# Optimization experiments

Measured on AMD Instinct MI355X. Metric: run time of the kernel, lower is better.

The kernel has to match this reference:

```python
import jax, jax.numpy as jnp
import numpy as np

B, N, D = 64, 128, 512
NEG = 1e30


def _gru_cell(x, h, Wi, Wh, bi, bh):
    # torch nn.GRUCell math
    gi = x @ Wi.T + bi  # (B, 3D)
    gh = h @ Wh.T + bh  # (B, 3D)
    ir, iz, inn = jnp.split(gi, 3, axis=-1)
    hr, hz, hn = jnp.split(gh, 3, axis=-1)
    r = jax.nn.sigmoid(ir + hr)
    z = jax.nn.sigmoid(iz + hz)
    n = jnp.tanh(inn + r * hn)
    return (1.0 - z) * n + z * h


def setup_inputs() -> dict:
    key = jax.random.key(0)
    ks = jax.random.split(key, 16)
    s = 1.0 / np.sqrt(D)
    u = lambda k, shape: jax.random.uniform(k, shape, jnp.float32, -s, s)
    adj = jax.random.randint(ks[13], (B, N, N), 0, 2, jnp.int32)
    adj = adj.at[:, :, 0].set(1)  # ensure each causal prefix has >=1 unmasked edge
    s_mask = jax.random.randint(ks[14], (B, N, N), 0, 2, jnp.int32)
    o_mask = 1 - s_mask
    return {
        "features": jax.random.normal(ks[0], (B, N, D), jnp.float32),
        "Wi_c": u(ks[1], (3 * D, D)),
        "Wh_c": u(ks[2], (3 * D, D)),
        "bi_c": u(ks[3], (3 * D,)),
        "bh_c": u(ks[4], (3 * D,)),
        "Wi_p": u(ks[5], (3 * D, D)),
        "Wh_p": u(ks[6], (3 * D, D)),
        "bi_p": u(ks[7], (3 * D,)),
        "bh_p": u(ks[8], (3 * D,)),
        "lin_w": u(ks[9], (1, 2 * D)),
        "lin_b": u(ks[10], (1,)),
        "Wr0": u(ks[11], (D, D)),
        "Wr1": u(ks[12], (D, D)),
        "adj": adj,
        "s_mask": s_mask,
        "o_mask": o_mask,
    }


def reference(features, Wi_c, Wh_c, bi_c, bh_c, Wi_p, Wh_p, bi_p, bh_p,
              lin_w, lin_b, Wr0, Wr1, adj, s_mask, o_mask):
    dt = features.dtype
    adj_f = adj.astype(dt)
    s_f = s_mask.astype(dt)
    o_f = o_mask.astype(dt)
    wq = lin_w[0, :D]   # applies to Q half of cat(Q, K)
    wk = lin_w[0, D:]   # applies to K half
    b = lin_b[0]
    pos = jnp.arange(N)

    # step 0
    x0 = features[:, 0]
    zeros = jnp.zeros((B, D), dt)
    C0 = _gru_cell(x0, zeros, Wi_c, Wh_c, bi_c, bh_c)
    P0 = _gru_cell(zeros, x0, Wi_p, Wh_p, bi_p, bh_p)
    H0 = jnp.zeros((B, N, D), dt).at[:, 0].set(C0 + P0)

    def step(H, inputs):
        i, x, adj_row, s_row, o_row = inputs
        # masked graph attention over the causal prefix [0, i)
        alpha = (x @ wq)[:, None] + H @ wk + b          # (B, N)
        valid = adj_row * (pos < i).astype(dt)          # (B, N)
        alpha = alpha - (1.0 - valid) * NEG
        w = jax.nn.softmax(alpha, axis=1)               # (B, N)
        V = (H @ Wr0.T) * s_row[:, :, None] + (H @ Wr1.T) * o_row[:, :, None]
        M = jnp.einsum('bn,bnd->bd', w, V)              # (B, D)
        C = _gru_cell(x, M, Wi_c, Wh_c, bi_c, bh_c)
        P = _gru_cell(M, x, Wi_p, Wh_p, bi_p, bh_p)
        H = H.at[:, i].set(C + P)
        return H, None

    xs = (jnp.arange(1, N),
          jnp.swapaxes(features, 0, 1)[1:],
          jnp.swapaxes(adj_f, 0, 1)[1:],
          jnp.swapaxes(s_f, 0, 1)[1:],
          jnp.swapaxes(o_f, 0, 1)[1:])
    H1, _ = jax.lax.scan(step, H0, xs)
    return H1
```

## Files before the change

kernel.cpp:

```cpp
#include <hip/hip_runtime.h>

#define BB 64
#define NN 128
#define DD 512
#define NBLK 128
#define NTHR 512
#define GCOLS 24
#define WCS 2064
#define WXS 1032
#define BCS 6656
#define UBE (BB * 2048)

typedef unsigned short u16;
typedef unsigned int u32;
typedef unsigned long long u64;
typedef __attribute__((ext_vector_type(8))) __bf16 bf16x8;
typedef __attribute__((ext_vector_type(4))) float f32x4;

#define MFMA16(a, b, c) __builtin_amdgcn_mfma_f32_16x16x32_bf16((a), (b), (c), 0, 0, 0)

__device__ __forceinline__ float b2f(u16 u) {
    union { u32 i; float f; } c; c.i = ((u32)u) << 16; return c.f;
}
__device__ __forceinline__ u16 f2b(float f) {
    union { float f; u32 i; } c; c.f = f;
    return (u16)((c.i + 0x7FFFu + ((c.i >> 16) & 1u)) >> 16);
}
__device__ __forceinline__ float sigm(float x) { return 1.f / (1.f + __expf(-x)); }
__device__ __forceinline__ float tanh_(float x) {
    x = fminf(fmaxf(x, -15.f), 15.f);
    float e = __expf(2.f * x);
    return (e - 1.f) / (e + 1.f);
}

__device__ __forceinline__ float ld_cohf(const float* p) {
    return __hip_atomic_load((float*)p, __ATOMIC_RELAXED, __HIP_MEMORY_SCOPE_AGENT);
}
__device__ __forceinline__ void st_cohf(float* p, float v) {
    __hip_atomic_store(p, v, __ATOMIC_RELAXED, __HIP_MEMORY_SCOPE_AGENT);
}
__device__ __forceinline__ void st_cohu32(u32* p, u32 v) {
    __hip_atomic_store(p, v, __ATOMIC_RELAXED, __HIP_MEMORY_SCOPE_AGENT);
}
__device__ __forceinline__ void st_cohi(int* p, int v) {
    __hip_atomic_store(p, v, __ATOMIC_RELAXED, __HIP_MEMORY_SCOPE_AGENT);
}
__device__ __forceinline__ int ld_cohi(int* p) {
    return __hip_atomic_load(p, __ATOMIC_RELAXED, __HIP_MEMORY_SCOPE_AGENT);
}

template<bool CACHED>
__device__ __forceinline__ bf16x8 ldu16(const u16* p) {
    if constexpr (CACHED) {
        return *(const bf16x8*)p;
    } else {
        union { bf16x8 v; u64 q[2]; } u;
        u.q[0] = __hip_atomic_load((u64*)p,     __ATOMIC_RELAXED, __HIP_MEMORY_SCOPE_AGENT);
        u.q[1] = __hip_atomic_load((u64*)p + 1, __ATOMIC_RELAXED, __HIP_MEMORY_SCOPE_AGENT);
        return u.v;
    }
}

__device__ __forceinline__ void gbar(int* sync, int gen, int blk) {
    __syncthreads();
    int* epoch = sync;
    if (blk == 0) {
        const int t = threadIdx.x;
        int done = (t == 0 || t >= NBLK) ? 1 : 0;
        int* myarr = sync + 256 + t * 16;
        int it = 0;
        for (;;) {
            if (!done) {
                int v = ((it & 15) == 15)
                    ? __hip_atomic_load(myarr, __ATOMIC_ACQUIRE, __HIP_MEMORY_SCOPE_AGENT)
                    : __hip_atomic_load(myarr, __ATOMIC_RELAXED, __HIP_MEMORY_SCOPE_AGENT);
                done = (v >= gen);
            }
            ++it;
            if (__syncthreads_and(done)) break;
            __builtin_amdgcn_s_sleep(1);
        }
        if (t == 0) {
            (void)__hip_atomic_load(sync + 256 + 16, __ATOMIC_ACQUIRE, __HIP_MEMORY_SCOPE_AGENT);
            __hip_atomic_store(epoch, gen, __ATOMIC_RELEASE, __HIP_MEMORY_SCOPE_AGENT);
        }
        __syncthreads();
    } else {
        if (threadIdx.x == 0) {
            __hip_atomic_store(sync + 256 + blk * 16, gen, __ATOMIC_RELEASE, __HIP_MEMORY_SCOPE_AGENT);
            int it = 0;
            for (;;) {
                int v = ((it & 15) == 15)
                    ? __hip_atomic_load(epoch, __ATOMIC_ACQUIRE, __HIP_MEMORY_SCOPE_AGENT)
                    : __hip_atomic_load(epoch, __ATOMIC_RELAXED, __HIP_MEMORY_SCOPE_AGENT);
                ++it;
                if (v >= gen) break;
                __builtin_amdgcn_s_sleep(1);
            }
            (void)__hip_atomic_load(epoch, __ATOMIC_ACQUIRE, __HIP_MEMORY_SCOPE_AGENT);
        }
        __syncthreads();
    }
}

__device__ __forceinline__ void gbar_lite(int* flags, int gen, int blk,
                                          int nsig, bool sig, bool wait) {
    __syncthreads();
    if (sig && threadIdx.x == 0)
        st_cohi(flags + blk * 32, gen);
    if (wait) {
        const int t = threadIdx.x;
        int done = (t >= nsig) ? 1 : 0;
        int* f = flags + t * 32;
        for (;;) {
            if (!done) done = (ld_cohi(f) >= gen);
            if (__syncthreads_and(done)) break;
            __builtin_amdgcn_s_sleep(2);
        }
    }
    asm volatile("" ::: "memory");
    __builtin_amdgcn_sched_barrier(0);
}

__device__ __forceinline__ void waitA(int* flagsA, int gen, int grp) {
    const int l = threadIdx.x & 63;
    int* f = flagsA + (grp * 16 + (l & 15)) * 32;
    for (;;) {
        int v = ld_cohi(f);
        if (__all(v >= gen)) break;
        __builtin_amdgcn_s_sleep(1);
    }
    asm volatile("" ::: "memory");
    __builtin_amdgcn_sched_barrier(0);
}

template<bool CACHED>
__device__ __forceinline__ void gates_merged(
    const u16* __restrict__ ub, const u16* s_wc, const float* s_gb,
    float* __restrict__ bc, int blk, int rt, int lr, int lq)
{
    const int cc0 = lr, cc1 = lr + 8;
    const u16* w0 = s_wc + cc0 * WCS;
    const u16* w1 = s_wc + cc1 * WCS;
    const u16* arow = ub + (size_t)(rt * 16 + lr) * 2048;
    f32x4 acc0 = {0.f, 0.f, 0.f, 0.f}, acc1 = {0.f, 0.f, 0.f, 0.f};
    #pragma unroll 4
    for (int c = 0; c < 16; ++c) {
        int kk = c * 32 + lq * 8;
        bf16x8 ah = ldu16<CACHED>(arow + kk);
        bf16x8 al = ldu16<CACHED>(arow + 512 + kk);
        bf16x8 wh0 = *(const bf16x8*)(w0 + kk);
        bf16x8 wl0 = *(const bf16x8*)(w0 + 1024 + kk);
        bf16x8 wh1 = *(const bf16x8*)(w1 + kk);
        bf16x8 wl1 = *(const bf16x8*)(w1 + 1024 + kk);
        acc0 = MFMA16(ah, wh0, acc0); acc0 = MFMA16(al, wh0, acc0); acc0 = MFMA16(ah, wl0, acc0);
        acc1 = MFMA16(ah, wh1, acc1); acc1 = MFMA16(al, wh1, acc1); acc1 = MFMA16(ah, wl1, acc1);
    }
    #pragma unroll 4
    for (int c = 0; c < 16; ++c) {
        int kk = c * 32 + lq * 8;
        bf16x8 ah = ldu16<CACHED>(arow + 1024 + kk);
        bf16x8 al = ldu16<CACHED>(arow + 1536 + kk);
        bf16x8 wh0 = *(const bf16x8*)(w0 + 512 + kk);
        bf16x8 wl0 = *(const bf16x8*)(w0 + 1536 + kk);
        bf16x8 wh1 = *(const bf16x8*)(w1 + 512 + kk);
        bf16x8 wl1 = *(const bf16x8*)(w1 + 1536 + kk);
        acc0 = MFMA16(ah, wh0, acc0); acc0 = MFMA16(al, wh0, acc0); acc0 = MFMA16(ah, wl0, acc0);
        acc1 = MFMA16(ah, wh1, acc1); acc1 = MFMA16(al, wh1, acc1); acc1 = MFMA16(ah, wl1, acc1);
    }
    float b0 = s_gb[cc0], b1 = s_gb[cc1];
    int col0 = blk * GCOLS + cc0, col1 = blk * GCOLS + cc1;
    #pragma unroll
    for (int r = 0; r < 4; ++r) {
        size_t row = (size_t)(rt * 16 + lq * 4 + r) * BCS;
        st_cohf(bc + row + 512 + col0, acc0[r] + b0);
        st_cohf(bc + row + 512 + col1, acc1[r] + b1);
    }
}

__device__ __forceinline__ f32x4 x_core(
    int i, const u16* __restrict__ featblob, const u16* s_wxw,
    int task, int lr, int lq, int* ccO)
{
    const int ct = task & 1, rt = task >> 1;
    const int cc = ct * 8 + lr;
    *ccO = cc;
    const u16* wcol = s_wxw + cc * WXS;
    const u16* arow = featblob + (size_t)(i * 64 + rt * 16 + lr) * 1024;
    f32x4 acc = {0.f, 0.f, 0.f, 0.f};
    #pragma unroll 4
    for (int c = 0; c < 16; ++c) {
        int kk = c * 32 + lq * 8;
        bf16x8 ah = *(const bf16x8*)(arow + kk);
        bf16x8 al = *(const bf16x8*)(arow + 512 + kk);
        bf16x8 wh = *(const bf16x8*)(wcol + kk);
        bf16x8 wl = *(const bf16x8*)(wcol + 512 + kk);
        acc = MFMA16(ah, wh, acc); acc = MFMA16(al, wh, acc); acc = MFMA16(ah, wl, acc);
    }
    return acc;
}

__device__ __forceinline__ void x_task(
    int i, const u16* __restrict__ featblob, const u16* s_wxw, const float* s_xb,
    float* __restrict__ bc, int blk, int task, int lr, int lq)
{
    int cc; f32x4 acc = x_core(i, featblob, s_wxw, task, lr, lq, &cc);
    const int rt = task >> 1;
    const int col = blk * GCOLS + cc;
    float bias = s_xb[cc];
    #pragma unroll
    for (int r = 0; r < 4; ++r)
        st_cohf(bc + (size_t)(rt * 16 + lq * 4 + r) * BCS + 3584 + col, acc[r] + bias);
}

__device__ __forceinline__ void x_task_xg(
    int i, const u16* __restrict__ featblob, const u16* s_wxw, const float* s_xb,
    float* __restrict__ xg, int blk, int task, int lr, int lq)
{
    int cc; f32x4 acc = x_core(i, featblob, s_wxw, task, lr, lq, &cc);
    const int rt = task >> 1;
    const int col = blk * GCOLS + cc;
    float bias = s_xb[cc];
    #pragma unroll
    for (int r = 0; r < 4; ++r)
        xg[((size_t)i * 64 + rt * 16 + lq * 4 + r) * 3072 + col] = acc[r] + bias;
}

template<bool CACHED>
__device__ __forceinline__ void m_task(
    const u16* __restrict__ ub, const u16* __restrict__ WrB,
    float* __restrict__ bc, int blk, int lr, int lq)
{
    const int ct = blk >> 2, rt = blk & 3;
    const int col = ct * 16 + lr;
    const u16* wcol = WrB + (size_t)col * 2048;
    const u16* arow = ub + (size_t)(rt * 16 + lr) * 2048;
    f32x4 acc = {0.f, 0.f, 0.f, 0.f};
    #pragma unroll 4
    for (int c = 0; c < 16; ++c) {
        int kk = c * 32 + lq * 8;
        bf16x8 a0h = ldu16<CACHED>(arow + kk);
        bf16x8 a0l = ldu16<CACHED>(arow + 512 + kk);
        bf16x8 a1h = ldu16<CACHED>(arow + 1024 + kk);
        bf16x8 a1l = ldu16<CACHED>(arow + 1536 + kk);
        bf16x8 w0h = *(const bf16x8*)(wcol + kk);
        bf16x8 w0l = *(const bf16x8*)(wcol + 512 + kk);
        bf16x8 w1h = *(const bf16x8*)(wcol + 1024 + kk);
        bf16x8 w1l = *(const bf16x8*)(wcol + 1536 + kk);
        acc = MFMA16(a0h, w0h, acc); acc = MFMA16(a0l, w0h, acc); acc = MFMA16(a0h, w0l, acc);
        acc = MFMA16(a1h, w1h, acc); acc = MFMA16(a1l, w1h, acc); acc = MFMA16(a1h, w1l, acc);
    }
    #pragma unroll
    for (int r = 0; r < 4; ++r)
        st_cohf(bc + (size_t)(rt * 16 + lq * 4 + r) * BCS + col, acc[r]);
}

__global__ __launch_bounds__(NTHR) void grn_kernel(
    const float* __restrict__ feat, const float* __restrict__ Wi_c, const float* __restrict__ Wh_c,
    const float* __restrict__ bi_c, const float* __restrict__ bh_c,
    const float* __restrict__ Wi_p, const float* __restrict__ Wh_p,
    const float* __restrict__ bi_p, const float* __restrict__ bh_p,
    const float* __restrict__ lin_w, const float* __restrict__ lin_b,
    const float* __restrict__ Wr0, const float* __restrict__ Wr1,
    const int* __restrict__ adj, const int* __restrict__ smask,
    float* __restrict__ out,
    float* __restrict__ q, u16* __restrict__ ublob,
    u16* __restrict__ featblob, float* __restrict__ bc, u16* __restrict__ WrB,
    float* __restrict__ xg, int* __restrict__ sync, int use_ring, int use_xg)
{
    const int t = threadIdx.x, blk = blockIdx.x;
    const int lane = t & 63, wv = t >> 6;
    const int lr = lane & 15, lq = lane >> 4;
    int gen = 0;
    int* flagsA = sync + 4096;
    int* flagsB = sync + 8192;

    __shared__ u16 s_wc[GCOLS * WCS];
    __shared__ __align__(16) char s_wx_raw[GCOLS * WXS * 2];
    __shared__ float s_u0[DD];
    __shared__ float s_ut[DD];
    __shared__ float s_red[NTHR];
    __shared__ float s_hk[NN];
    __shared__ float s_q[NN];
    __shared__ float s_w[NN];
    __shared__ float s_ws[NN];
    __shared__ float s_gb[GCOLS];
    __shared__ float s_xb[GCOLS];

    u16* s_wxw = (u16*)s_wx_raw;
    float* s_wgf = (float*)s_wx_raw;
    float* s_pu = (float*)s_wx_raw;
    float* s_pt = (float*)(s_wx_raw + 6144);
    float* s_scal = (float*)(s_wx_raw + 12288);

    const float wkreg = lin_w[DD + t];

    for (int rr = 0; rr < 64; ++rr) {
        int gr = blk * 64 + rr;
        int bb_ = gr >> 7, nn_ = gr & 127;
        float x = feat[(size_t)gr * DD + t];
        u16 h = f2b(x);
        u16* dst = featblob + (size_t)(nn_ * 64 + bb_) * 1024;
        dst[t] = h;
        dst[512 + t] = f2b(x - b2f(h));
    }
    for (int cc = 0; cc < 4; ++cc) {
        int c = blk * 4 + cc;
        float w0 = Wr0[(size_t)c * DD + t], w1 = Wr1[(size_t)c * DD + t];
        u16 h0 = f2b(w0), h1 = f2b(w1);
        u16* dst = WrB + (size_t)c * 2048;
        dst[t] = h0; dst[512 + t] = f2b(w0 - b2f(h0));
        dst[1024 + t] = h1; dst[1536 + t] = f2b(w1 - b2f(h1));
    }
    {
        float linb = lin_b[0];
        float wqf[8];
        #pragma unroll
        for (int jj = 0; jj < 8; ++jj) wqf[jj] = lin_w[lane * 8 + jj];
        for (int rr = 0; rr < 8; ++rr) {
            int row = blk * 64 + wv * 8 + rr;
            const float* fp = feat + (size_t)row * DD + lane * 8;
            float p = 0.f;
            #pragma unroll
            for (int jj = 0; jj < 8; ++jj) p += fp[jj] * wqf[jj];
            #pragma unroll
            for (int off = 32; off; off >>= 1) p += __shfl_down(p, off, 64);
            if (lane == 0) q[row] = p + linb;
        }
    }
    {
        int jg0 = blk * GCOLS;
        for (int cc = 0; cc < GCOLS; ++cc) {
            int jg = jg0 + cc;
            const float* src = (jg < 1536) ? (Wh_c + (size_t)jg * DD) : (Wi_p + (size_t)(jg - 1536) * DD);
            s_wgf[t * GCOLS + cc] = src[t];
        }
        if (t < GCOLS) {
            int jg = jg0 + t;
            s_gb[t] = (jg < 1536) ? bh_c[jg] : bi_p[jg - 1536];
            s_xb[t] = (jg < 1536) ? bi_c[jg] : bh_p[jg - 1536];
        }
    }
    __syncthreads();
    {
        float acc0[GCOLS], acc1[GCOLS];
        #pragma unroll
        for (int cc = 0; cc < GCOLS; ++cc) { acc0[cc] = 0.f; acc1[cc] = 0.f; }
        for (int j = 0; j < DD; ++j) {
            float wr0 = Wr0[(size_t)j * DD + t];
            float wr1 = Wr1[(size_t)j * DD + t];
            const float* g = s_wgf + j * GCOLS;
            #pragma unroll
            for (int cc = 0; cc < GCOLS; ++cc) {
                float gv = g[cc];
                acc0[cc] += wr0 * gv;
                acc1[cc] += wr1 * gv;
            }
        }
        __syncthreads();
        #pragma unroll
        for (int cc = 0; cc < GCOLS; ++cc) {
            u16 h0 = f2b(acc0[cc]);
            s_wc[cc * WCS + t] = h0;
            s_wc[cc * WCS + 1024 + t] = f2b(acc0[cc] - b2f(h0));
            u16 h1 = f2b(acc1[cc]);
            s_wc[cc * WCS + 512 + t] = h1;
            s_wc[cc * WCS + 1536 + t] = f2b(acc1[cc] - b2f(h1));
        }
    }
    {
        int jx0 = blk * GCOLS;
        for (int cc = 0; cc < GCOLS; ++cc) {
            int jx = jx0 + cc;
            const float* src = (jx < 1536) ? (Wi_c + (size_t)jx * DD) : (Wh_p + (size_t)(jx - 1536) * DD);
            float w = src[t];
            u16 h = f2b(w);
            s_wxw[cc * WXS + t] = h;
            s_wxw[cc * WXS + 512 + t] = f2b(w - b2f(h));
        }
    }
    gbar(sync, ++gen, blk);

    x_task(0, featblob, s_wxw, s_xb, bc, blk, wv, lr, lq);
    if (use_xg) {
        for (int ii = 0; ii < NN; ++ii)
            x_task_xg(ii, featblob, s_wxw, s_xb, xg, blk, wv, lr, lq);
    }
    if (blk < BB && t < NN) s_q[t] = q[blk * NN + t];
    gbar(sync, ++gen, blk);

    if (blk < BB) {
        if (use_xg) {
            s_pu[t] = 0.f; s_pu[512 + t] = 0.f; s_pu[1024 + t] = 0.f;
            s_pt[t] = 0.f; s_pt[512 + t] = 0.f; s_pt[1024 + t] = 0.f;
            if (t == 0) {
                s_scal[0] = -1e30f; s_scal[1] = 0.f;
                s_scal[2] = (float)adj[((size_t)blk * NN + 1) * NN + 0];
                s_scal[3] = (float)smask[((size_t)blk * NN + 1) * NN + 0];
            }
        }
        const float* bcb = bc + (size_t)blk * BCS;
        float ir = ld_cohf(bcb + 3584 + t), iz = ld_cohf(bcb + 4096 + t), inn = ld_cohf(bcb + 4608 + t);
        float r = sigm(ir + bh_c[t]), z = sigm(iz + bh_c[512 + t]);
        float C = (1.f - z) * tanh_(inn + r * bh_c[1024 + t]);
        float ghr = ld_cohf(bcb + 5120 + t), ghz = ld_cohf(bcb + 5632 + t), ghn = ld_cohf(bcb + 6144 + t);
        float r2 = sigm(bi_p[t] + ghr), z2 = sigm(bi_p[512 + t] + ghz);
        float n2 = tanh_(bi_p[1024 + t] + r2 * ghn);
        float x = feat[(size_t)(blk * NN) * DD + t];
        float P = (1.f - z2) * n2 + z2 * x;
        float Hv = C + P;
        out[(size_t)(blk * NN) * DD + t] = Hv;
        s_red[t] = Hv * wkreg;
        __syncthreads();
        if (wv == 0) {
            float p = 0.f;
            #pragma unroll
            for (int jj = 0; jj < 8; ++jj) p += s_red[lane + 64 * jj];
            #pragma unroll
            for (int off = 32; off; off >>= 1) p += __shfl_down(p, off, 64);
            if (lane == 0) s_hk[0] = p;
        }
    }
    gbar(sync, ++gen, blk);

    for (int i = 1; i < NN; ++i) {
        u16* ub_i = ublob + (size_t)(use_ring ? (NN - 1 - i) : 0) * UBE;

        if (blk < BB) {
            if (use_xg) {
                int j = i - 1;
                float Hv;
                if (i >= 2) {
                    const float* bcb = bc + (size_t)blk * BCS;
                    float Mv = ld_cohf(bcb + t);
                    float hr = ld_cohf(bcb + 512 + t), hz = ld_cohf(bcb + 1024 + t), hn = ld_cohf(bcb + 1536 + t);
                    float gir = ld_cohf(bcb + 2048 + t), giz = ld_cohf(bcb + 2560 + t), gin = ld_cohf(bcb + 3072 + t);
                    const float* xrow = xg + ((size_t)j * 64 + blk) * 3072;
                    float ir = xrow[t], iz = xrow[512 + t], inn = xrow[1024 + t];
                    float ghr = xrow[1536 + t], ghz = xrow[2048 + t], ghn = xrow[2560 + t];
                    float x = feat[(size_t)(blk * NN + j) * DD + t];
                    float r = sigm(ir + hr), z = sigm(iz + hz);
                    float C = (1.f - z) * tanh_(inn + r * hn) + z * Mv;
                    float r2 = sigm(gir + ghr), z2 = sigm(giz + ghz);
                    float P = (1.f - z2) * tanh_(gin + r2 * ghn) + z2 * x;
                    Hv = C + P;
                    out[(size_t)(blk * NN + j) * DD + t] = Hv;
                    s_red[t] = Hv * wkreg;
                } else {
                    Hv = out[(size_t)(blk * NN) * DD + t];
                }
                __syncthreads();
                if (wv == 0) {
                    float hk;
                    if (i >= 2) {
                        float p = 0.f;
                        #pragma unroll
                        for (int jj = 0; jj < 8; ++jj) p += s_red[lane + 64 * jj];
                        #pragma unroll
                        for (int off = 32; off; off >>= 1) p += __shfl_down(p, off, 64);
                        if (lane == 0) s_hk[j] = p;
                        hk = p;
                    } else {
                        hk = s_hk[0];
                    }
                    if (lane == 0) {
                        float m_part = s_scal[0], denom_p = s_scal[1];
                        float anew = s_scal[2], snew = s_scal[3];
                        float alpha = s_q[i] + hk;
                        float m = m_part, e_new = 0.f;
                        if (anew != 0.f) { m = fmaxf(m_part, alpha); e_new = __expf(alpha - m); }
                        float scale = __expf(m_part - m);
                        float inv = 1.f / (denom_p * scale + e_new);
                        s_w[0] = scale * inv;
                        s_w[1] = e_new * snew * inv;
                        s_w[2] = e_new * inv;
                    }
                }
                __syncthreads();
                {
                    float u0p = s_pu[t] + s_pu[512 + t] + s_pu[1024 + t];
                    float utp = s_pt[t] + s_pt[512 + t] + s_pt[1024 + t];
                    float CS = s_w[0], C0 = s_w[1], CT = s_w[2];
                    float U0 = u0p * CS + C0 * Hv;
                    float U1 = (utp * CS + CT * Hv) - U0;
                    u16 h0 = f2b(U0); u16 l0 = f2b(U0 - b2f(h0));
                    u16 h1 = f2b(U1); u16 l1 = f2b(U1 - b2f(h1));
                    u32 p0 = (u32)h0 | ((u32)l0 << 16);
                    u32 p1 = (u32)h1 | ((u32)l1 << 16);
                    u32 q0 = (u32)__shfl_xor((int)p0, 1, 64);
                    u32 q1 = (u32)__shfl_xor((int)p1, 1, 64);
                    u32* ub32 = (u32*)(ub_i + (size_t)blk * 2048);
                    int w = t >> 1;
                    if ((t & 1) == 0) {
                        st_cohu32(ub32 + w,       (p0 & 0xFFFFu) | ((q0 & 0xFFFFu) << 16));
                        st_cohu32(ub32 + 256 + w, (p0 >> 16)     | (q0 & 0xFFFF0000u));
                    } else {
                        st_cohu32(ub32 + 512 + w, (q1 & 0xFFFFu) | ((p1 & 0xFFFFu) << 16));
                        st_cohu32(ub32 + 768 + w, (q1 >> 16)     | (p1 & 0xFFFF0000u));
                    }
                }
                __syncthreads();
                if (t == 0) st_cohi(flagsA + blk * 32, i);
            } else {
                int va0 = 0, va1 = 0, vs0 = 0, vs1 = 0;
                float qv = 0.f;
                if (wv == 0) {
                    const int* ar_ = adj + (size_t)(blk * NN + i) * NN;
                    const int* sr_ = smask + (size_t)(blk * NN + i) * NN;
                    va0 = ar_[lane]; va1 = ar_[lane + 64];
                    vs0 = sr_[lane]; vs1 = sr_[lane + 64];
                    qv = s_q[i];
                }
                if (i >= 2) {
                    int j = i - 1;
                    const float* bcb = bc + (size_t)blk * BCS;
                    float Mv = ld_cohf(bcb + t);
                    float hr = ld_cohf(bcb + 512 + t), hz = ld_cohf(bcb + 1024 + t), hn = ld_cohf(bcb + 1536 + t);
                    float gir = ld_cohf(bcb + 2048 + t), giz = ld_cohf(bcb + 2560 + t), gin = ld_cohf(bcb + 3072 + t);
                    float ir = ld_cohf(bcb + 3584 + t), iz = ld_cohf(bcb + 4096 + t), inn = ld_cohf(bcb + 4608 + t);
                    float ghr = ld_cohf(bcb + 5120 + t), ghz = ld_cohf(bcb + 5632 + t), ghn = ld_cohf(bcb + 6144 + t);
                    float x = feat[(size_t)(blk * NN + j) * DD + t];
                    float r = sigm(ir + hr), z = sigm(iz + hz);
                    float C = (1.f - z) * tanh_(inn + r * hn) + z * Mv;
                    float r2 = sigm(gir + ghr), z2 = sigm(giz + ghz);
                    float P = (1.f - z2) * tanh_(gin + r2 * ghn) + z2 * x;
                    float Hv = C + P;
                    out[(size_t)(blk * NN + j) * DD + t] = Hv;
                    s_red[t] = Hv * wkreg;
                }
                s_u0[t] = 0.f; s_ut[t] = 0.f;
                __syncthreads();
                if (wv == 0) {
                    if (i >= 2) {
                        float p = 0.f;
                        #pragma unroll
                        for (int jj = 0; jj < 8; ++jj) p += s_red[lane + 64 * jj];
                        #pragma unroll
                        for (int off = 32; off; off >>= 1) p += __shfl_down(p, off, 64);
                        if (lane == 0) s_hk[i - 1] = p;
                    }
                    int n2i = lane + 64;
                    float a0 = (lane < i && va0 != 0) ? (qv + s_hk[lane]) : -1e30f;
                    float a1 = (n2i < i && va1 != 0) ? (qv + s_hk[n2i]) : -1e30f;
                    float m = fmaxf(a0, a1);
                    #pragma unroll
                    for (int off = 32; off; off >>= 1) m = fmaxf(m, __shfl_xor(m, off, 64));
                    float e0 = (a0 > -1e29f) ? __expf(a0 - m) : 0.f;
                    float e1 = (a1 > -1e29f) ? __expf(a1 - m) : 0.f;
                    float ss = e0 + e1;
                    #pragma unroll
                    for (int off = 32; off; off >>= 1) ss += __shfl_xor(ss, off, 64);
                    float inv = 1.f / ss;
                    float w0 = e0 * inv, w1 = e1 * inv;
                    s_w[lane] = w0; s_w[n2i] = w1;
                    s_ws[lane] = w0 * (float)vs0;
                    s_ws[n2i] = w1 * (float)vs1;
                }
                __syncthreads();
                {
                    int g = t >> 7, dqb = (t & 127) * 4;
                    const float* Hb = out + (size_t)blk * NN * DD + dqb;
                    f32x4 u0 = {0.f, 0.f, 0.f, 0.f}, ut = {0.f, 0.f, 0.f, 0.f};
                    int n = g;
                    for (; n + 12 < i; n += 16) {
                        f32x4 h0 = *(const f32x4*)(Hb + (size_t)n * DD);
                        f32x4 h1 = *(const f32x4*)(Hb + (size_t)(n + 4) * DD);
                        f32x4 h2 = *(const f32x4*)(Hb + (size_t)(n + 8) * DD);
                        f32x4 h3 = *(const f32x4*)(Hb + (size_t)(n + 12) * DD);
                        u0 += s_ws[n] * h0 + s_ws[n + 4] * h1 + s_ws[n + 8] * h2 + s_ws[n + 12] * h3;
                        ut += s_w[n] * h0 + s_w[n + 4] * h1 + s_w[n + 8] * h2 + s_w[n + 12] * h3;
                    }
                    for (; n < i; n += 4) {
                        f32x4 h0 = *(const f32x4*)(Hb + (size_t)n * DD);
                        u0 += s_ws[n] * h0;
                        ut += s_w[n] * h0;
                    }
                    #pragma unroll
                    for (int e = 0; e < 4; ++e) {
                        atomicAdd(&s_u0[dqb + e], u0[e]);
                        atomicAdd(&s_ut[dqb + e], ut[e]);
                    }
                }
                __syncthreads();
                {
                    int tt = t & 255, sel = t >> 8;
                    float a0 = s_u0[2 * tt], a1 = s_u0[2 * tt + 1];
                    float t0_ = s_ut[2 * tt], t1_ = s_ut[2 * tt + 1];
                    float b0_ = t0_ - a0, b1_ = t1_ - a1;
                    float v0 = sel ? b0_ : a0, v1 = sel ? b1_ : a1;
                    u16 h0 = f2b(v0), h1 = f2b(v1);
                    u16 l0 = f2b(v0 - b2f(h0)), l1 = f2b(v1 - b2f(h1));
                    u32 hw = (u32)h0 | ((u32)h1 << 16);
                    u32 lw = (u32)l0 | ((u32)l1 << 16);
                    u32* ub32 = (u32*)(ub_i + (size_t)blk * 2048);
                    int base = sel * 512;
                    st_cohu32(ub32 + base + tt, hw);
                    st_cohu32(ub32 + base + 256 + tt, lw);
                }
                __syncthreads();
                if (t == 0) st_cohi(flagsA + blk * 32, i);
            }
        }

        if (use_xg) {
            if (wv < 4) {
                waitA(flagsA, i, wv);
                if (use_ring) gates_merged<true >(ub_i, s_wc, s_gb, bc, blk, wv, lr, lq);
                else          gates_merged<false>(ub_i, s_wc, s_gb, bc, blk, wv, lr, lq);
            } else if (wv == 7) {
                waitA(flagsA, i, blk & 3);
                if (use_ring) m_task<true >(ub_i, WrB, bc, blk, lr, lq);
                else          m_task<false>(ub_i, WrB, bc, blk, lr, lq);
            } else if (blk < BB && i + 1 < NN) {
                const int ii = i + 1;
                const int w = wv - 4;
                const int* ar = adj + (size_t)(blk * NN + ii) * NN;
                const int* sr = smask + (size_t)(blk * NN + ii) * NN;
                int a0 = ar[lane], a1 = ar[lane + 64];
                int s0 = sr[lane], s1 = sr[lane + 64];
                float qv = s_q[ii];
                float al0 = (lane < i && a0 != 0) ? (qv + s_hk[lane]) : -1e30f;
                float al1 = (lane + 64 < i && a1 != 0) ? (qv + s_hk[lane + 64]) : -1e30f;
                float m = fmaxf(al0, al1);
                #pragma unroll
                for (int off = 32; off; off >>= 1) m = fmaxf(m, __shfl_xor(m, off, 64));
                float e0 = (al0 > -1e29f) ? __expf(al0 - m) : 0.f;
                float e1 = (al1 > -1e29f) ? __expf(al1 - m) : 0.f;
                float es0 = e0 * (float)s0, es1 = e1 * (float)s1;
                const float* Hb = out + (size_t)blk * NN * DD + lane * 8;
                f32x4 pa = {0.f,0.f,0.f,0.f}, pb = {0.f,0.f,0.f,0.f};
                f32x4 ta = {0.f,0.f,0.f,0.f}, tb = {0.f,0.f,0.f,0.f};
                for (int n = w; n < i; n += 3) {
                    float en  = __shfl((n < 64) ? e0 : e1, n & 63, 64);
                    float esn = __shfl((n < 64) ? es0 : es1, n & 63, 64);
                    f32x4 h0 = *(const f32x4*)(Hb + (size_t)n * DD);
                    f32x4 h1 = *(const f32x4*)(Hb + (size_t)n * DD + 4);
                    pa += esn * h0; pb += esn * h1;
                    ta += en * h0;  tb += en * h1;
                }
                *(f32x4*)&s_pu[w * 512 + lane * 8]     = pa;
                *(f32x4*)&s_pu[w * 512 + lane * 8 + 4] = pb;
                *(f32x4*)&s_pt[w * 512 + lane * 8]     = ta;
                *(f32x4*)&s_pt[w * 512 + lane * 8 + 4] = tb;
                if (w == 0) {
                    float ds = e0 + e1;
                    #pragma unroll
                    for (int off = 32; off; off >>= 1) ds += __shfl_xor(ds, off, 64);
                    if (lane == 0) {
                        s_scal[0] = m; s_scal[1] = ds;
                        s_scal[2] = (float)ar[i];
                        s_scal[3] = (float)sr[i];
                    }
                }
                if (w == 2) {
                    const float* fp = feat + (size_t)(blk * NN + i) * DD + lane * 8;
                    f32x4 f0 = *(const f32x4*)fp;
                    f32x4 f1 = *(const f32x4*)(fp + 4);
                    const float* xp = xg + ((size_t)i * 64 + blk) * 3072 + lane * 16;
                    float x0 = xp[0], x1 = xp[1024], x2 = xp[2048];
                    asm volatile("" :: "v"(f0), "v"(f1), "v"(x0), "v"(x1), "v"(x2));
                }
            }
        } else {
            if (wv < 4) {
                waitA(flagsA, i, wv);
                gates_merged<false>(ub_i, s_wc, s_gb, bc, blk, wv, lr, lq);
            } else if (wv == 4) {
                x_task(i, featblob, s_wxw, s_xb, bc, blk, 0, lr, lq);
                x_task(i, featblob, s_wxw, s_xb, bc, blk, 1, lr, lq);
                x_task(i, featblob, s_wxw, s_xb, bc, blk, 2, lr, lq);
            } else if (wv == 5) {
                x_task(i, featblob, s_wxw, s_xb, bc, blk, 3, lr, lq);
                x_task(i, featblob, s_wxw, s_xb, bc, blk, 4, lr, lq);
                x_task(i, featblob, s_wxw, s_xb, bc, blk, 5, lr, lq);
            } else if (wv == 6) {
                x_task(i, featblob, s_wxw, s_xb, bc, blk, 6, lr, lq);
                x_task(i, featblob, s_wxw, s_xb, bc, blk, 7, lr, lq);
            } else {
                waitA(flagsA, i, blk & 3);
                m_task<false>(ub_i, WrB, bc, blk, lr, lq);
            }
        }

        gbar_lite(flagsB, i, blk, NBLK, true, blk < BB);
    }

    if (blk < BB) {
        int j = NN - 1;
        const float* bcb = bc + (size_t)blk * BCS;
        float Mv = ld_cohf(bcb + t);
        float hr = ld_cohf(bcb + 512 + t), hz = ld_cohf(bcb + 1024 + t), hn = ld_cohf(bcb + 1536 + t);
        float gir = ld_cohf(bcb + 2048 + t), giz = ld_cohf(bcb + 2560 + t), gin = ld_cohf(bcb + 3072 + t);
        float ir, iz, inn, ghr, ghz, ghn;
        if (use_xg) {
            const float* xrow = xg + ((size_t)j * 64 + blk) * 3072;
            ir = xrow[t]; iz = xrow[512 + t]; inn = xrow[1024 + t];
            ghr = xrow[1536 + t]; ghz = xrow[2048 + t]; ghn = xrow[2560 + t];
        } else {
            ir = ld_cohf(bcb + 3584 + t); iz = ld_cohf(bcb + 4096 + t); inn = ld_cohf(bcb + 4608 + t);
            ghr = ld_cohf(bcb + 5120 + t); ghz = ld_cohf(bcb + 5632 + t); ghn = ld_cohf(bcb + 6144 + t);
        }
        float x = feat[(size_t)(blk * NN + j) * DD + t];
        float r = sigm(ir + hr), z = sigm(iz + hz);
        float C = (1.f - z) * tanh_(inn + r * hn) + z * Mv;
        float r2 = sigm(gir + ghr), z2 = sigm(giz + ghz);
        float P = (1.f - z2) * tanh_(gin + r2 * ghn) + z2 * x;
        out[(size_t)(blk * NN + j) * DD + t] = C + P;
    }
}

extern "C" void kernel_launch(void* const* d_in, const int* in_sizes, int n_in,
                              void* d_out, int out_size, void* d_ws, size_t ws_size,
                              hipStream_t stream) {
    (void)in_sizes; (void)n_in; (void)out_size;
    const float* feat = (const float*)d_in[0];
    const float* Wi_c = (const float*)d_in[1];
    const float* Wh_c = (const float*)d_in[2];
    const float* bi_c = (const float*)d_in[3];
    const float* bh_c = (const float*)d_in[4];
    const float* Wi_p = (const float*)d_in[5];
    const float* Wh_p = (const float*)d_in[6];
    const float* bi_p = (const float*)d_in[7];
    const float* bh_p = (const float*)d_in[8];
    const float* lin_w = (const float*)d_in[9];
    const float* lin_b = (const float*)d_in[10];
    const float* Wr0 = (const float*)d_in[11];
    const float* Wr1 = (const float*)d_in[12];
    const int* adj = (const int*)d_in[13];
    const int* smask = (const int*)d_in[14];
    float* out = (float*)d_out;

    char* ws = (char*)d_ws;
    size_t off = 0;
    int* sync_ = (int*)(ws + off);      off += 65536;
    float* q = (float*)(ws + off);      off += (size_t)BB * NN * 4;
    u16* featblob = (u16*)(ws + off);   off += (size_t)BB * NN * 1024 * 2;
    float* bc = (float*)(ws + off);     off += (size_t)BB * BCS * 4;
    u16* WrB = (u16*)(ws + off);        off += (size_t)512 * 2048 * 2;
    u16* ublob = (u16*)(ws + off);
    size_t ring_bytes = (size_t)(NN - 1) * UBE * 2;
    size_t xg_bytes = (size_t)NN * 64 * 3072 * 4;
    int use_ring = (ws_size >= off + ring_bytes) ? 1 : 0;
    float* xg = (float*)(ws + off + ring_bytes);
    int use_xg = (use_ring && ws_size >= off + ring_bytes + xg_bytes) ? 1 : 0;

    (void)hipMemsetAsync(d_ws, 0, 65536, stream);
    hipLaunchKernelGGL(grn_kernel, dim3(NBLK), dim3(NTHR), 0, stream,
                       feat, Wi_c, Wh_c, bi_c, bh_c, Wi_p, Wh_p, bi_p, bh_p,
                       lin_w, lin_b, Wr0, Wr1, adj, smask, out,
                       q, ublob, featblob, bc, WrB, xg, sync_, use_ring, use_xg);
}
```

Baseline: 3.418 ms.

## Replace per-step grid barrier with per-wave completion counters and flag waits

On the precomputed-x path, the end-of-step grid barrier is removed. Each gate/M wave now bumps a shared-memory counter after its stores drain, and the last of the five raises a per-block flag. Consumer blocks wait at the start of the next step until all 128 producer flags reach the previous step. This lets the attention-prep waves of the next step overlap with other waves still running gate work, and cuts full-barrier overhead. The cost is more complex memory-ordering and flag logic, plus a risk of races if the counter thresholds or visibility are wrong.

After: 3.419 ms. About the same (+0.0%).

```diff
diff --git a/kernel.cpp b/kernel.cpp
--- a/kernel.cpp
+++ b/kernel.cpp
@@ -134,6 +134,15 @@
     __builtin_amdgcn_sched_barrier(0);
 }
 
+__device__ __forceinline__ void sigB(int* flagsB, int* sd, int i, int blk, int lane) {
+    asm volatile("s_waitcnt vmcnt(0)" ::: "memory");
+    if (lane == 0) {
+        int old = atomicAdd(sd, 1);
+        if (old == 5 * i - 1)
+            st_cohi(flagsB + blk * 32, i);
+    }
+}
+
 template<bool CACHED>
 __device__ __forceinline__ void gates_merged(
     const u16* __restrict__ ub, const u16* s_wc, const float* s_gb,
@@ -143,7 +152,7 @@
     const u16* w0 = s_wc + cc0 * WCS;
     const u16* w1 = s_wc + cc1 * WCS;
     const u16* arow = ub + (size_t)(rt * 16 + lr) * 2048;
-    f32x4 acc0 = {0.f, 0.f, 0.f, 0.f}, acc1 = {0.f, 0.f, 0.f, 0.f};
+    f32x4 acc0 = {0.f,0.f,0.f,0.f}, acc1 = {0.f,0.f,0.f,0.f};
     #pragma unroll 4
     for (int c = 0; c < 16; ++c) {
         int kk = c * 32 + lq * 8;
@@ -187,7 +196,7 @@
     *ccO = cc;
     const u16* wcol = s_wxw + cc * WXS;
     const u16* arow = featblob + (size_t)(i * 64 + rt * 16 + lr) * 1024;
-    f32x4 acc = {0.f, 0.f, 0.f, 0.f};
+    f32x4 acc = {0.f,0.f,0.f,0.f};
     #pragma unroll 4
     for (int c = 0; c < 16; ++c) {
         int kk = c * 32 + lq * 8;
@@ -235,7 +244,7 @@
     const int col = ct * 16 + lr;
     const u16* wcol = WrB + (size_t)col * 2048;
     const u16* arow = ub + (size_t)(rt * 16 + lr) * 2048;
-    f32x4 acc = {0.f, 0.f, 0.f, 0.f};
+    f32x4 acc = {0.f,0.f,0.f,0.f};
     #pragma unroll 4
     for (int c = 0; c < 16; ++c) {
         int kk = c * 32 + lq * 8;
@@ -286,6 +295,7 @@
     __shared__ float s_ws[NN];
     __shared__ float s_gb[GCOLS];
     __shared__ float s_xb[GCOLS];
+    __shared__ int s_done;
 
     u16* s_wxw = (u16*)s_wx_raw;
     float* s_wgf = (float*)s_wx_raw;
@@ -421,13 +431,29 @@
             if (lane == 0) s_hk[0] = p;
         }
     }
+    if (t == 0) s_done = 0;
     gbar(sync, ++gen, blk);
 
     for (int i = 1; i < NN; ++i) {
         u16* ub_i = ublob + (size_t)(use_ring ? (NN - 1 - i) : 0) * UBE;
 
-        if (blk < BB) {
-            if (use_xg) {
+        if (use_xg) {
+            if (blk < BB) {
+                if (i >= 2) {
+                    if (wv == 0) {
+                        int* fa = flagsB + lane * 32;
+                        int* fb = flagsB + (lane + 64) * 32;
+                        for (;;) {
+                            int va = ld_cohi(fa);
+                            int vb = ld_cohi(fb);
+                            if (__all((va >= i - 1) && (vb >= i - 1))) break;
+                            __builtin_amdgcn_s_sleep(1);
+                        }
+                        asm volatile("" ::: "memory");
+                        __builtin_amdgcn_sched_barrier(0);
+                    }
+                    __syncthreads();
+                }
                 int j = i - 1;
                 float Hv;
                 if (i >= 2) {
@@ -501,7 +527,82 @@
                 }
                 __syncthreads();
                 if (t == 0) st_cohi(flagsA + blk * 32, i);
+
+                if (wv < 4) {
+                    waitA(flagsA, i, wv);
+                    if (use_ring) gates_merged<true >(ub_i, s_wc, s_gb, bc, blk, wv, lr, lq);
+                    else          gates_merged<false>(ub_i, s_wc, s_gb, bc, blk, wv, lr, lq);
+                    sigB(flagsB, &s_done, i, blk, lane);
+                } else if (wv == 7) {
+                    waitA(flagsA, i, blk & 3);
+                    if (use_ring) m_task<true >(ub_i, WrB, bc, blk, lr, lq);
+                    else          m_task<false>(ub_i, WrB, bc, blk, lr, lq);
+                    sigB(flagsB, &s_done, i, blk, lane);
+                } else if (i + 1 < NN) {
+                    const int ii = i + 1;
+                    const int w = wv - 4;
+                    const int* ar = adj + (size_t)(blk * NN + ii) * NN;
+                    const int* sr = smask + (size_t)(blk * NN + ii) * NN;
+                    int a0 = ar[lane], a1 = ar[lane + 64];
+                    int s0 = sr[lane], s1 = sr[lane + 64];
+                    float qv = s_q[ii];
+                    float al0 = (lane < i && a0 != 0) ? (qv + s_hk[lane]) : -1e30f;
+                    float al1 = (lane + 64 < i && a1 != 0) ? (qv + s_hk[lane + 64]) : -1e30f;
+                    float m = fmaxf(al0, al1);
+                    #pragma unroll
+                    for (int off = 32; off; off >>= 1) m = fmaxf(m, __shfl_xor(m, off, 64));
+                    float e0 = (al0 > -1e29f) ? __expf(al0 - m) : 0.f;
+                    float e1 = (al1 > -1e29f) ? __expf(al1 - m) : 0.f;
+                    float es0 = e0 * (float)s0, es1 = e1 * (float)s1;
+                    const float* Hb = out + (size_t)blk * NN * DD + lane * 8;
+                    f32x4 pa = {0.f,0.f,0.f,0.f}, pb = {0.f,0.f,0.f,0.f};
+                    f32x4 ta = {0.f,0.f,0.f,0.f}, tb = {0.f,0.f,0.f,0.f};
+                    for (int n = w; n < i; n += 3) {
+                        float en  = __shfl((n < 64) ? e0 : e1, n & 63, 64);
+                        float esn = __shfl((n < 64) ? es0 : es1, n & 63, 64);
+                        f32x4 h0 = *(const f32x4*)(Hb + (size_t)n * DD);
+                        f32x4 h1 = *(const f32x4*)(Hb + (size_t)n * DD + 4);
+                        pa += esn * h0; pb += esn * h1;
+                        ta += en * h0;  tb += en * h1;
+                    }
+                    *(f32x4*)&s_pu[w * 512 + lane * 8]     = pa;
+                    *(f32x4*)&s_pu[w * 512 + lane * 8 + 4] = pb;
+                    *(f32x4*)&s_pt[w * 512 + lane * 8]     = ta;
+                    *(f32x4*)&s_pt[w * 512 + lane * 8 + 4] = tb;
+                    if (w == 0) {
+                        float ds = e0 + e1;
+                        #pragma unroll
+                        for (int off = 32; off; off >>= 1) ds += __shfl_xor(ds, off, 64);
+                        if (lane == 0) {
+                            s_scal[0] = m; s_scal[1] = ds;
+                            s_scal[2] = (float)ar[i];
+                            s_scal[3] = (float)sr[i];
+                        }
+                    }
+                    if (w == 2) {
+                        const float* fp = feat + (size_t)(blk * NN + i) * DD + lane * 8;
+                        f32x4 f0 = *(const f32x4*)fp;
+                        f32x4 f1 = *(const f32x4*)(fp + 4);
+                        const float* xp = xg + ((size_t)i * 64 + blk) * 3072 + lane * 16;
+                        float x0 = xp[0], x1 = xp[1024], x2 = xp[2048];
+                        asm volatile("" :: "v"(f0), "v"(f1), "v"(x0), "v"(x1), "v"(x2));
+                    }
+                }
             } else {
+                if (wv < 4) {
+                    waitA(flagsA, i, wv);
+                    if (use_ring) gates_merged<true >(ub_i, s_wc, s_gb, bc, blk, wv, lr, lq);
+                    else          gates_merged<false>(ub_i, s_wc, s_gb, bc, blk, wv, lr, lq);
+                    sigB(flagsB, &s_done, i, blk, lane);
+                } else if (wv == 7) {
+                    waitA(flagsA, i, blk & 3);
+                    if (use_ring) m_task<true >(ub_i, WrB, bc, blk, lr, lq);
+                    else          m_task<false>(ub_i, WrB, bc, blk, lr, lq);
+                    sigB(flagsB, &s_done, i, blk, lane);
+                }
+            }
+        } else {
+            if (blk < BB) {
                 int va0 = 0, va1 = 0, vs0 = 0, vs1 = 0;
                 float qv = 0.f;
                 if (wv == 0) {
@@ -560,7 +661,7 @@
                 {
                     int g = t >> 7, dqb = (t & 127) * 4;
                     const float* Hb = out + (size_t)blk * NN * DD + dqb;
-                    f32x4 u0 = {0.f, 0.f, 0.f, 0.f}, ut = {0.f, 0.f, 0.f, 0.f};
+                    f32x4 u0 = {0.f,0.f,0.f,0.f}, ut = {0.f,0.f,0.f,0.f};
                     int n = g;
                     for (; n + 12 < i; n += 16) {
                         f32x4 h0 = *(const f32x4*)(Hb + (size_t)n * DD);
@@ -600,68 +701,6 @@
                 __syncthreads();
                 if (t == 0) st_cohi(flagsA + blk * 32, i);
             }
-        }
-
-        if (use_xg) {
-            if (wv < 4) {
-                waitA(flagsA, i, wv);
-                if (use_ring) gates_merged<true >(ub_i, s_wc, s_gb, bc, blk, wv, lr, lq);
-                else          gates_merged<false>(ub_i, s_wc, s_gb, bc, blk, wv, lr, lq);
-            } else if (wv == 7) {
-                waitA(flagsA, i, blk & 3);
-                if (use_ring) m_task<true >(ub_i, WrB, bc, blk, lr, lq);
-                else          m_task<false>(ub_i, WrB, bc, blk, lr, lq);
-            } else if (blk < BB && i + 1 < NN) {
-                const int ii = i + 1;
-                const int w = wv - 4;
-                const int* ar = adj + (size_t)(blk * NN + ii) * NN;
-                const int* sr = smask + (size_t)(blk * NN + ii) * NN;
-                int a0 = ar[lane], a1 = ar[lane + 64];
-                int s0 = sr[lane], s1 = sr[lane + 64];
-                float qv = s_q[ii];
-                float al0 = (lane < i && a0 != 0) ? (qv + s_hk[lane]) : -1e30f;
-                float al1 = (lane + 64 < i && a1 != 0) ? (qv + s_hk[lane + 64]) : -1e30f;
-                float m = fmaxf(al0, al1);
-                #pragma unroll
-                for (int off = 32; off; off >>= 1) m = fmaxf(m, __shfl_xor(m, off, 64));
-                float e0 = (al0 > -1e29f) ? __expf(al0 - m) : 0.f;
-                float e1 = (al1 > -1e29f) ? __expf(al1 - m) : 0.f;
-                float es0 = e0 * (float)s0, es1 = e1 * (float)s1;
-                const float* Hb = out + (size_t)blk * NN * DD + lane * 8;
-                f32x4 pa = {0.f,0.f,0.f,0.f}, pb = {0.f,0.f,0.f,0.f};
-                f32x4 ta = {0.f,0.f,0.f,0.f}, tb = {0.f,0.f,0.f,0.f};
-                for (int n = w; n < i; n += 3) {
-                    float en  = __shfl((n < 64) ? e0 : e1, n & 63, 64);
-                    float esn = __shfl((n < 64) ? es0 : es1, n & 63, 64);
-                    f32x4 h0 = *(const f32x4*)(Hb + (size_t)n * DD);
-                    f32x4 h1 = *(const f32x4*)(Hb + (size_t)n * DD + 4);
-                    pa += esn * h0; pb += esn * h1;
-                    ta += en * h0;  tb += en * h1;
-                }
-                *(f32x4*)&s_pu[w * 512 + lane * 8]     = pa;
-                *(f32x4*)&s_pu[w * 512 + lane * 8 + 4] = pb;
-                *(f32x4*)&s_pt[w * 512 + lane * 8]     = ta;
-                *(f32x4*)&s_pt[w * 512 + lane * 8 + 4] = tb;
-                if (w == 0) {
-                    float ds = e0 + e1;
-                    #pragma unroll
-                    for (int off = 32; off; off >>= 1) ds += __shfl_xor(ds, off, 64);
-                    if (lane == 0) {
-                        s_scal[0] = m; s_scal[1] = ds;
-                        s_scal[2] = (float)ar[i];
-                        s_scal[3] = (float)sr[i];
-                    }
-                }
-                if (w == 2) {
-                    const float* fp = feat + (size_t)(blk * NN + i) * DD + lane * 8;
-                    f32x4 f0 = *(const f32x4*)fp;
-                    f32x4 f1 = *(const f32x4*)(fp + 4);
-                    const float* xp = xg + ((size_t)i * 64 + blk) * 3072 + lane * 16;
-                    float x0 = xp[0], x1 = xp[1024], x2 = xp[2048];
-                    asm volatile("" :: "v"(f0), "v"(f1), "v"(x0), "v"(x1), "v"(x2));
-                }
-            }
-        } else {
             if (wv < 4) {
                 waitA(flagsA, i, wv);
                 gates_merged<false>(ub_i, s_wc, s_gb, bc, blk, wv, lr, lq);
@@ -680,12 +719,26 @@
                 waitA(flagsA, i, blk & 3);
                 m_task<false>(ub_i, WrB, bc, blk, lr, lq);
             }
-        }
-
-        gbar_lite(flagsB, i, blk, NBLK, true, blk < BB);
+            gbar_lite(flagsB, i, blk, NBLK, true, blk < BB);
+        }
     }
 
     if (blk < BB) {
+        if (use_xg) {
+            if (wv == 0) {
+                int* fa = flagsB + lane * 32;
+                int* fb = flagsB + (lane + 64) * 32;
+                for (;;) {
+                    int va = ld_cohi(fa);
+                    int vb = ld_cohi(fb);
+                    if (__all((va >= NN - 1) && (vb >= NN - 1))) break;
+                    __builtin_amdgcn_s_sleep(1);
+                }
+                asm volatile("" ::: "memory");
+                __builtin_amdgcn_sched_barrier(0);
+            }
+            __syncthreads();
+        }
         int j = NN - 1;
         const float* bcb = bc + (size_t)blk * BCS;
         float Mv = ld_cohf(bcb + t);
```
